# Performance work log

Measured on AMD Instinct MI355X. Metric: run time of the kernel, lower is better.

Reference implementation:

```python
import jax, jax.numpy as jnp
import numpy as np

B, T, V = 16, 512, 10000
E, H = 300, 256


def setup_inputs() -> dict:
    key = jax.random.key(0)
    ks = jax.random.split(key, 6)
    return {
        "input": jax.random.normal(ks[0], (B, T, V), dtype=jnp.float32),
        "hidden": jax.random.normal(ks[1], (B, H), dtype=jnp.float32),
        "W_emb": jax.random.normal(ks[2], (E, V), dtype=jnp.float32) * 0.02,
        "W_w": jax.random.normal(ks[3], (H, E), dtype=jnp.float32) * 0.05,
        "W_u": jax.random.normal(ks[4], (H, H), dtype=jnp.float32) * 0.05,
        "W_v": jax.random.normal(ks[5], (V, H), dtype=jnp.float32) * 0.05,
    }


def reference(input, hidden, W_emb, W_w, W_u, W_v):
    # Elman-style cell WITHOUT nonlinearity on the hidden state (matches source):
    #   e = x_t @ W_emb^T ; h = e @ W_w^T + h_prev @ W_u^T ; out = softmax(h @ W_v^T)
    def step(h, x_t):  # x_t: [B, V], h: [B, H]
        e = x_t @ W_emb.T                      # [B, E]
        h_new = e @ W_w.T + h @ W_u.T          # [B, H]
        out = jax.nn.softmax(h_new @ W_v.T, axis=1)  # [B, V]
        return h_new, out

    xs = jnp.swapaxes(input, 0, 1)             # [T, B, V]
    _, outs = jax.lax.scan(step, hidden, xs)   # outs: [T, B, V]
    return jnp.swapaxes(outs, 0, 1)            # [B, T, V]
```

## Files before the change

### kernel.cpp

```cpp
#include <hip/hip_runtime.h>

typedef __bf16 bf16x8 __attribute__((ext_vector_type(8)));
typedef float f32x4 __attribute__((ext_vector_type(4)));
typedef unsigned short u16x8 __attribute__((ext_vector_type(8)));

#define VP 10016

__device__ __forceinline__ unsigned short f2bf(float x){
  unsigned u = __builtin_bit_cast(unsigned, x);
  u += 0x7fffu + ((u>>16)&1u);
  return (unsigned short)(u>>16);
}
__device__ __forceinline__ float bf2f(unsigned short h){
  unsigned u = ((unsigned)h)<<16;
  return __builtin_bit_cast(float, u);
}

__global__ __launch_bounds__(256) void k_wvf(const float* __restrict__ W_v,
                                             unsigned short* __restrict__ Wvf,
                                             const float* __restrict__ W_u,
                                             unsigned short* __restrict__ Wu_bf){
  if(blockIdx.x >= 160){
    int i = (blockIdx.x-160)*256 + threadIdx.x;
    const float4 v = *(const float4*)(W_u + (size_t)i*4);
    unsigned a = (unsigned)f2bf(v.x) | ((unsigned)f2bf(v.y)<<16);
    unsigned b = (unsigned)f2bf(v.z) | ((unsigned)f2bf(v.w)<<16);
    *(uint2*)(Wu_bf + (size_t)i*4) = make_uint2(a,b);
    return;
  }
  const int t = threadIdx.x;
  const int w = t>>6, lane = t&63;
  const int l15 = lane&15, sl = lane>>4;
  const int vg = blockIdx.x*4 + w;
  const int v = vg*16 + l15;
  #pragma unroll
  for(int kk=0;kk<8;kk++){
    u16x8 pk = {0,0,0,0,0,0,0,0};
    if(v < 10000){
      const float* p = W_v + (size_t)v*256 + kk*32 + sl*8;
      float4 v0 = *(const float4*)p;
      float4 v1 = *(const float4*)(p+4);
      pk[0]=f2bf(v0.x); pk[1]=f2bf(v0.y); pk[2]=f2bf(v0.z); pk[3]=f2bf(v0.w);
      pk[4]=f2bf(v1.x); pk[5]=f2bf(v1.y); pk[6]=f2bf(v1.z); pk[7]=f2bf(v1.w);
    }
    *(u16x8*)(Wvf + ((size_t)vg*8 + kk)*512 + lane*8) = pk;
  }
}

__global__ __launch_bounds__(256) void k_m1(const float* __restrict__ W_w,
                                            const float* __restrict__ W_emb,
                                            unsigned short* __restrict__ M1f){
  __shared__ float4 ww4[16][75];
  const int t = threadIdx.x;
  const int ngrp = blockIdx.y;
  const int n0 = ngrp*16;
  for(int i=t; i<16*75; i+=256){
    int n = i/75, c = i - n*75;
    ww4[n][c] = *(const float4*)(W_w + (size_t)(n0+n)*300 + c*4);
  }
  __syncthreads();
  const int v0 = blockIdx.x*512 + t*2;
  if(v0 >= VP) return;
  const int c  = v0>>5;
  const int sl = (v0>>3)&3;
  const int j  = v0&7;
  unsigned short* outp = M1f + (size_t)(ngrp*313 + c)*512 + sl*128 + j;
  if(v0 >= 10000){
    #pragma unroll
    for(int nn=0;nn<16;nn++) *(unsigned*)&outp[nn*8] = 0u;
    return;
  }
  float acc[16][2];
  #pragma unroll
  for(int nn=0;nn<16;nn++){ acc[nn][0]=0.f; acc[nn][1]=0.f; }
  #pragma unroll 2
  for(int cc=0;cc<75;cc++){
    const float* eb = W_emb + (size_t)(4*cc)*10000 + v0;
    float2 wv0 = *(const float2*)(eb);
    float2 wv1 = *(const float2*)(eb + 10000);
    float2 wv2 = *(const float2*)(eb + 20000);
    float2 wv3 = *(const float2*)(eb + 30000);
    #pragma unroll
    for(int nn=0;nn<16;nn++){
      float4 w = ww4[nn][cc];
      acc[nn][0] += w.x*wv0.x + w.y*wv1.x + w.z*wv2.x + w.w*wv3.x;
      acc[nn][1] += w.x*wv0.y + w.y*wv1.y + w.z*wv2.y + w.w*wv3.y;
    }
  }
  #pragma unroll
  for(int nn=0;nn<16;nn++){
    unsigned pk = (unsigned)f2bf(acc[nn][0]) | ((unsigned)f2bf(acc[nn][1])<<16);
    *(unsigned*)&outp[nn*8] = pk;
  }
}

__global__ __launch_bounds__(512, 4) void k_gemm_a(const float* __restrict__ x,
    const unsigned short* __restrict__ M1f, float* __restrict__ gp, int nsplit){
  __shared__ unsigned short As[32768];
  char* Ab = (char*)As;
  const int t = threadIdx.x;
  const int w = t>>6, lane = t&63;
  const int l15 = lane&15, sl = lane>>4;
  const int mh = w>>2, nq = w&3;
  const int r0 = blockIdx.x*128;
  const int kh = blockIdx.y;
  const int base = 313/nsplit, rem = 313%nsplit;
  const int c0 = kh*base + (kh<rem ? kh : rem);
  const int c1 = c0 + base + (kh<rem ? 1 : 0);

  const unsigned short* mbp[4];
  #pragma unroll
  for(int nt=0;nt<4;nt++)
    mbp[nt] = M1f + (size_t)(nq*4+nt)*313*512 + lane*8;

  f32x4 acc[4][4] = {};
  for(int cs=c0; cs<c1; cs+=8){
    const int cs_n = (c1-cs) < 8 ? (c1-cs) : 8;
    if(lane*4 < cs_n*32){
      const int kk = cs*32 + lane*4;
      const bool ok = (kk + 4 <= 10000);
      const int unit0 = lane>>1;
      const int half8 = (lane&1)*8;
      const float* xp = x + (size_t)(r0 + w*16)*10000 + kk;
      #pragma unroll
      for(int g=0; g<2; g++){
        float4 rX[8];
        #pragma unroll
        for(int j=0;j<8;j++)
          rX[j] = ok ? *(const float4*)(xp + (size_t)(g*8+j)*10000)
                     : float4{0.f,0.f,0.f,0.f};
        #pragma unroll
        for(int j=0;j<8;j++){
          const int r = w*16 + g*8 + j;
          unsigned lo = (unsigned)f2bf(rX[j].x) | ((unsigned)f2bf(rX[j].y)<<16);
          unsigned hi = (unsigned)f2bf(rX[j].z) | ((unsigned)f2bf(rX[j].w)<<16);
          *(uint2*)(Ab + r*512 + (((lane>>1) ^ (r&7))<<4) + half8) = make_uint2(lo,hi);
        }
      }
      (void)unit0;
    }
    __syncthreads();
    for(int cc=0; cc<cs_n; cc++){
      const int c = cs + cc;
      bf16x8 b[4];
      #pragma unroll
      for(int nt=0;nt<4;nt++)
        b[nt] = *(const bf16x8*)(mbp[nt] + (size_t)c*512);
      bf16x8 a[4];
      #pragma unroll
      for(int mt=0;mt<4;mt++){
        const int r = mh*64 + mt*16 + l15;
        const int p = (cc*4 + sl) ^ (l15&7);
        a[mt] = *(const bf16x8*)(Ab + r*512 + p*16);
      }
      #pragma unroll
      for(int mt=0;mt<4;mt++)
        #pragma unroll
        for(int nt=0;nt<4;nt++)
          acc[mt][nt] = __builtin_amdgcn_mfma_f32_16x16x32_bf16(a[mt], b[nt], acc[mt][nt], 0,0,0);
    }
    __syncthreads();
  }

  float* gout = gp + (size_t)kh*2097152;
  #pragma unroll
  for(int mt=0;mt<4;mt++)
    #pragma unroll
    for(int nt=0;nt<4;nt++)
      #pragma unroll
      for(int i2=0;i2<4;i2++){
        int row = r0 + mh*64 + mt*16 + sl*4 + i2;
        int col = nq*64 + nt*16 + l15;
        gout[(size_t)row*256 + col] = acc[mt][nt][i2];
      }
}

__global__ __launch_bounds__(256) void k_reduce(float* __restrict__ gp, int nsplit){
  size_t i = ((size_t)blockIdx.x*256 + threadIdx.x)*4;
  float4 acc = *(const float4*)(gp + i);
  for(int s=1;s<nsplit;s++){
    const float4 v = *(const float4*)(gp + (size_t)s*2097152 + i);
    acc.x+=v.x; acc.y+=v.y; acc.z+=v.z; acc.w+=v.w;
  }
  *(float4*)(gp + i) = acc;
}

__global__ __launch_bounds__(256) void k_matsq(const float* __restrict__ A,
    const float* __restrict__ B, float* __restrict__ C){
  int i = blockIdx.x, j = threadIdx.x;
  __shared__ float arow[256];
  arow[j] = A[i*256 + j];
  __syncthreads();
  float acc = 0.f;
  for(int k=0;k<256;k++) acc += arow[k]*B[k*256 + j];
  C[i*256 + j] = acc;
}

__global__ __launch_bounds__(256) void k_scan_local(const float* __restrict__ g,
    const unsigned short* __restrict__ Wu, float* __restrict__ u_final){
  __shared__ unsigned short ub[2][16*256];
  const int m = blockIdx.x;
  const int t = threadIdx.x, wave=t>>6, lane=t&63, l15=lane&15, sl=lane>>4;
  for(int i=t;i<2048;i+=256) ((unsigned*)ub[0])[i] = 0u;
  __syncthreads();
  int buf = 0;
  for(int j=0;j<16;j++){
    float gv[4][4];
    #pragma unroll
    for(int nt=0;nt<4;nt++)
      #pragma unroll
      for(int i=0;i<4;i++){
        int b = sl*4 + i;
        int n = wave*64 + nt*16 + l15;
        size_t r = (size_t)b*512 + m*16 + j;
        gv[nt][i] = g[r*256 + n];
      }
    bf16x8 af[8];
    #pragma unroll
    for(int kk=0;kk<8;kk++){
      int slot = kk*4 + sl;
      af[kk] = *(const bf16x8*)&ub[buf][l15*256 + ((slot ^ (l15&7))<<3)];
    }
    f32x4 acc[4] = {};
    #pragma unroll
    for(int kk=0;kk<8;kk++)
      #pragma unroll
      for(int nt=0;nt<4;nt++){
        int n = wave*64 + nt*16 + l15;
        bf16x8 bv = *(const bf16x8*)&Wu[(size_t)n*256 + kk*32 + sl*8];
        acc[nt] = __builtin_amdgcn_mfma_f32_16x16x32_bf16(af[kk], bv, acc[nt], 0,0,0);
      }
    #pragma unroll
    for(int nt=0;nt<4;nt++)
      #pragma unroll
      for(int i=0;i<4;i++){
        int b = sl*4 + i;
        int n = wave*64 + nt*16 + l15;
        float v = acc[nt][i] + gv[nt][i];
        ub[buf^1][b*256 + (((n>>3) ^ (b&7))<<3) + (n&7)] = f2bf(v);
        if(j==15) u_final[m*4096 + b*256 + n] = v;
      }
    __syncthreads();
    buf ^= 1;
  }
}

__global__ __launch_bounds__(1024) void k_chunk_scan(const float* __restrict__ hidden,
    const float* __restrict__ u_final, const float* __restrict__ A16,
    float* __restrict__ h_start){
  const int b = blockIdx.x;
  const int t = threadIdx.x;
  const int n = t & 255, q = t >> 8;
  __shared__ float hc[256];
  __shared__ float part[3][256];
  float a[64];
  const float* ap = A16 + (size_t)n*256 + q*64;
  #pragma unroll
  for(int i=0;i<16;i++){
    float4 v = *(const float4*)(ap + i*4);
    a[i*4]=v.x; a[i*4+1]=v.y; a[i*4+2]=v.z; a[i*4+3]=v.w;
  }
  if(q==0){
    float h = hidden[b*256 + n];
    hc[n] = h;
    h_start[b*256 + n] = h;
  }
  __syncthreads();
  for(int m=1;m<32;m++){
    float acc0=0.f, acc1=0.f;
    #pragma unroll
    for(int i=0;i<64;i+=2){
      acc0 += a[i]  *hc[q*64 + i];
      acc1 += a[i+1]*hc[q*64 + i+1];
    }
    float acc = acc0 + acc1;
    if(q) part[q-1][n] = acc;
    __syncthreads();
    if(q==0){
      float v = acc + part[0][n] + part[1][n] + part[2][n]
              + u_final[(size_t)(m-1)*4096 + b*256 + n];
      hc[n] = v;
      h_start[(size_t)m*4096 + b*256 + n] = v;
    }
    __syncthreads();
  }
}

__global__ __launch_bounds__(256) void k_scan_fix(const float* __restrict__ g,
    const unsigned short* __restrict__ Wu, const float* __restrict__ h_start,
    unsigned short* __restrict__ h_bf){
  __shared__ unsigned short ub[2][16*256];
  const int m = blockIdx.x;
  const int t=threadIdx.x, wave=t>>6, lane=t&63, l15=lane&15, sl=lane>>4;
  for(int u=t; u<512; u+=256){
    int b = u>>5, s = u&31;
    const float* hp = h_start + m*4096 + b*256 + s*8;
    float4 v0 = *(const float4*)hp;
    float4 v1 = *(const float4*)(hp+4);
    u16x8 pk;
    pk[0]=f2bf(v0.x); pk[1]=f2bf(v0.y); pk[2]=f2bf(v0.z); pk[3]=f2bf(v0.w);
    pk[4]=f2bf(v1.x); pk[5]=f2bf(v1.y); pk[6]=f2bf(v1.z); pk[7]=f2bf(v1.w);
    *(u16x8*)&ub[0][b*256 + ((s ^ (b&7))<<3)] = pk;
  }
  __syncthreads();
  int buf = 0;
  for(int j=0;j<16;j++){
    float gv[4][4];
    #pragma unroll
    for(int nt=0;nt<4;nt++)
      #pragma unroll
      for(int i=0;i<4;i++){
        int b = sl*4 + i;
        int n = wave*64 + nt*16 + l15;
        size_t r = (size_t)b*512 + m*16 + j;
        gv[nt][i] = g[r*256 + n];
      }
    bf16x8 af[8];
    #pragma unroll
    for(int kk=0;kk<8;kk++){
      int slot = kk*4 + sl;
      af[kk] = *(const bf16x8*)&ub[buf][l15*256 + ((slot ^ (l15&7))<<3)];
    }
    f32x4 acc[4] = {};
    #pragma unroll
    for(int kk=0;kk<8;kk++)
      #pragma unroll
      for(int nt=0;nt<4;nt++){
        int n = wave*64 + nt*16 + l15;
        bf16x8 bv = *(const bf16x8*)&Wu[(size_t)n*256 + kk*32 + sl*8];
        acc[nt] = __builtin_amdgcn_mfma_f32_16x16x32_bf16(af[kk], bv, acc[nt], 0,0,0);
      }
    #pragma unroll
    for(int nt=0;nt<4;nt++)
      #pragma unroll
      for(int i=0;i<4;i++){
        int b = sl*4 + i;
        int n = wave*64 + nt*16 + l15;
        float v = acc[nt][i] + gv[nt][i];
        unsigned short hb = f2bf(v);
        ub[buf^1][b*256 + (((n>>3) ^ (b&7))<<3) + (n&7)] = hb;
        size_t r = (size_t)b*512 + m*16 + j;
        h_bf[r*256 + n] = hb;
      }
    __syncthreads();
    buf ^= 1;
  }
}

__global__ __launch_bounds__(512, 2) void k_gemm_c(const unsigned short* __restrict__ h_bf,
    const unsigned short* __restrict__ Wvf, char* __restrict__ out){
  const int t = threadIdx.x;
  const int w = t>>6, lane = t&63;
  const int l15 = lane&15, sl = lane>>4;
  const int mh = w>>2, nq = w&3;
  const int vt = blockIdx.x;

  const unsigned short* bp[4];
  #pragma unroll
  for(int nt=0;nt<4;nt++)
    bp[nt] = Wvf + (size_t)(vt*16 + nq*4 + nt)*8*512 + lane*8;

  bf16x8 ball[8][4];
  #pragma unroll
  for(int kk=0;kk<8;kk++)
    #pragma unroll
    for(int nt=0;nt<4;nt++)
      ball[kk][nt] = *(const bf16x8*)(bp[nt] + (size_t)kk*512);

  #pragma unroll
  for(int band=0; band<2; band++){
    const int rg = blockIdx.y + band*32;
    const int rbase = rg*128 + mh*64;
    f32x4 acc[4][4] = {};
    #pragma unroll
    for(int kk=0;kk<8;kk++){
      bf16x8 a[4];
      #pragma unroll
      for(int mt=0;mt<4;mt++)
        a[mt] = *(const bf16x8*)&h_bf[(size_t)(rbase + mt*16 + l15)*256 + kk*32 + sl*8];
      #pragma unroll
      for(int mt=0;mt<4;mt++)
        #pragma unroll
        for(int nt=0;nt<4;nt++)
          acc[mt][nt] = __builtin_amdgcn_mfma_f32_16x16x32_bf16(a[mt], ball[kk][nt], acc[mt][nt], 0,0,0);
    }
    #pragma unroll
    for(int mt=0;mt<4;mt++)
      #pragma unroll
      for(int nt=0;nt<4;nt++){
        const int v = vt*256 + (nq*4+nt)*16 + l15;
        if(v < 10000){
          #pragma unroll
          for(int i=0;i<4;i++){
            int row = rbase + mt*16 + sl*4 + i;
            *(unsigned short*)(out + (size_t)row*40000 + (size_t)v*2) = f2bf(acc[mt][nt][i]);
          }
        }
      }
  }
}

__global__ __launch_bounds__(256) void k_softmax(char* __restrict__ out){
  const int r = blockIdx.x;
  const int t = threadIdx.x;
  const unsigned short* lg = (const unsigned short*)(out + (size_t)r*40000);
  float vals[40];
  float mx = -3.0e38f;
  #pragma unroll
  for(int j=0;j<5;j++){
    int c = j*256 + t;
    if(c < 1250){
      u16x8 p = *(const u16x8*)(lg + (size_t)c*8);
      #pragma unroll
      for(int q=0;q<8;q++){
        float a = bf2f(p[q]);
        vals[j*8+q] = a;
        mx = fmaxf(mx, a);
      }
    }
  }
  #pragma unroll
  for(int o=32;o>=1;o>>=1) mx = fmaxf(mx, __shfl_xor(mx, o));
  __shared__ float redm[4], reds[4];
  if((t&63)==0) redm[t>>6] = mx;
  __syncthreads();
  mx = fmaxf(fmaxf(redm[0],redm[1]), fmaxf(redm[2],redm[3]));
  float s = 0.f;
  #pragma unroll
  for(int j=0;j<5;j++){
    int c = j*256 + t;
    if(c < 1250){
      #pragma unroll
      for(int q=0;q<8;q++){
        float e = __expf(vals[j*8+q]-mx);
        vals[j*8+q] = e;
        s += e;
      }
    }
  }
  #pragma unroll
  for(int o=32;o>=1;o>>=1) s += __shfl_xor(s, o);
  if((t&63)==0) reds[t>>6] = s;
  __syncthreads();
  s = reds[0]+reds[1]+reds[2]+reds[3];
  float inv = 1.0f/s;
  float* op = (float*)(out + (size_t)r*40000);
  #pragma unroll
  for(int j=0;j<5;j++){
    int c = j*256 + t;
    if(c < 1250){
      float4 s0, s1;
      s0.x=vals[j*8+0]*inv; s0.y=vals[j*8+1]*inv; s0.z=vals[j*8+2]*inv; s0.w=vals[j*8+3]*inv;
      s1.x=vals[j*8+4]*inv; s1.y=vals[j*8+5]*inv; s1.z=vals[j*8+6]*inv; s1.w=vals[j*8+7]*inv;
      *(float4*)(op + (size_t)c*8)     = s0;
      *(float4*)(op + (size_t)c*8 + 4) = s1;
    }
  }
}

extern "C" void kernel_launch(void* const* d_in, const int* in_sizes, int n_in,
                              void* d_out, int out_size, void* d_ws, size_t ws_size,
                              hipStream_t stream){
  const float* x      = (const float*)d_in[0];
  const float* hidden = (const float*)d_in[1];
  const float* W_emb  = (const float*)d_in[2];
  const float* W_w    = (const float*)d_in[3];
  const float* W_u    = (const float*)d_in[4];
  const float* W_v    = (const float*)d_in[5];

  const size_t fixed_bytes = 16269312;
  int nsplit = 2;
  if(ws_size >= (size_t)8*2097152*4 + fixed_bytes) nsplit = 8;
  else if(ws_size >= (size_t)4*2097152*4 + fixed_bytes) nsplit = 4;

  char* w = (char*)d_ws;
  size_t off = (size_t)nsplit * 2097152 * 4;
  float*          gp      = (float*)(w + 0);
  unsigned short* M1f     = (unsigned short*)(w + off);          off += 5128192;
  unsigned short* Wvf     = (unsigned short*)(w + off);          off += 5242880;
  unsigned short* Wu_bf   = (unsigned short*)(w + off);          off += 131072;
  float*          u_final = (float*)(w + off);                   off += 524288;
  float*          h_start = (float*)(w + off);                   off += 524288;
  unsigned short* h_bf    = (unsigned short*)(w + off);          off += 4194304;
  float*          powA    = (float*)(w + off);                   off += 262144;
  float*          powB    = (float*)(w + off);                   off += 262144;

  k_m1<<<dim3(20,16),256,0,stream>>>(W_w, W_emb, M1f);
  k_gemm_a<<<dim3(64,nsplit),512,0,stream>>>(x, M1f, gp, nsplit);
  k_wvf<<<224,256,0,stream>>>(W_v, Wvf, W_u, Wu_bf);
  k_matsq<<<256,256,0,stream>>>(W_u,  W_u,  powA);
  k_matsq<<<256,256,0,stream>>>(powA, powA, powB);
  k_matsq<<<256,256,0,stream>>>(powB, powB, powA);
  k_matsq<<<256,256,0,stream>>>(powA, powA, powB);
  k_reduce<<<2048,256,0,stream>>>(gp, nsplit);
  k_scan_local<<<32,256,0,stream>>>(gp, Wu_bf, u_final);
  k_chunk_scan<<<16,1024,0,stream>>>(hidden, u_final, powB, h_start);
  k_scan_fix<<<32,256,0,stream>>>(gp, Wu_bf, h_start, h_bf);
  k_gemm_c<<<dim3(40,32),512,0,stream>>>(h_bf, Wvf, (char*)d_out);
  k_softmax<<<8192,256,0,stream>>>((char*)d_out);
}
```

Before: 509.4 us.

## Double-buffer A tile in k_gemm_a with register prefetch of next chunk

Switches the GEMM's shared-memory A tile from one 8-chunk buffer to two 4-chunk buffers. Global loads for the next half-step are issued into registers before the MFMA loop over the current buffer, then converted and written to the alternate buffer. This removes one barrier per iteration and overlaps global-load latency with compute. The cost is twice as many loop iterations with smaller steps and more live registers, which may pressure occupancy at the 512x4 launch bound.

```diff
diff --git a/kernel.cpp b/kernel.cpp
--- a/kernel.cpp
+++ b/kernel.cpp
@@ -96,8 +96,7 @@
 
 __global__ __launch_bounds__(512, 4) void k_gemm_a(const float* __restrict__ x,
     const unsigned short* __restrict__ M1f, float* __restrict__ gp, int nsplit){
-  __shared__ unsigned short As[32768];
-  char* Ab = (char*)As;
+  __shared__ unsigned short As[2][16384];
   const int t = threadIdx.x;
   const int w = t>>6, lane = t&63;
   const int l15 = lane&15, sl = lane>>4;
@@ -113,35 +112,53 @@
   for(int nt=0;nt<4;nt++)
     mbp[nt] = M1f + (size_t)(nq*4+nt)*313*512 + lane*8;
 
+  const int lhalf = lane>>5, lcol = lane&31;
+  const float* xrow = x + (size_t)(r0 + w*16)*10000;
+  float4 rX[8];
+
+  auto LOADG = [&](int ch, int hn){
+    if(lcol < hn*8){
+      const int kk = ch*32 + lcol*4;
+      const bool ok = (kk + 4 <= 10000);
+      #pragma unroll
+      for(int jj=0;jj<8;jj++)
+        rX[jj] = ok ? *(const float4*)(xrow + (size_t)(2*jj+lhalf)*10000 + kk)
+                    : float4{0.f,0.f,0.f,0.f};
+    }
+  };
+  auto WRITEG = [&](int hn, int bufi){
+    if(lcol < hn*8){
+      char* Ab = (char*)As[bufi];
+      #pragma unroll
+      for(int jj=0;jj<8;jj++){
+        const int r = w*16 + 2*jj + lhalf;
+        unsigned lo = (unsigned)f2bf(rX[jj].x) | ((unsigned)f2bf(rX[jj].y)<<16);
+        unsigned hi = (unsigned)f2bf(rX[jj].z) | ((unsigned)f2bf(rX[jj].w)<<16);
+        *(uint2*)(Ab + r*256 + (((lcol>>1) ^ (r&7))<<4) + (lcol&1)*8) = make_uint2(lo,hi);
+      }
+    }
+  };
+
   f32x4 acc[4][4] = {};
-  for(int cs=c0; cs<c1; cs+=8){
-    const int cs_n = (c1-cs) < 8 ? (c1-cs) : 8;
-    if(lane*4 < cs_n*32){
-      const int kk = cs*32 + lane*4;
-      const bool ok = (kk + 4 <= 10000);
-      const int unit0 = lane>>1;
-      const int half8 = (lane&1)*8;
-      const float* xp = x + (size_t)(r0 + w*16)*10000 + kk;
-      #pragma unroll
-      for(int g=0; g<2; g++){
-        float4 rX[8];
-        #pragma unroll
-        for(int j=0;j<8;j++)
-          rX[j] = ok ? *(const float4*)(xp + (size_t)(g*8+j)*10000)
-                     : float4{0.f,0.f,0.f,0.f};
-        #pragma unroll
-        for(int j=0;j<8;j++){
-          const int r = w*16 + g*8 + j;
-          unsigned lo = (unsigned)f2bf(rX[j].x) | ((unsigned)f2bf(rX[j].y)<<16);
-          unsigned hi = (unsigned)f2bf(rX[j].z) | ((unsigned)f2bf(rX[j].w)<<16);
-          *(uint2*)(Ab + r*512 + (((lane>>1) ^ (r&7))<<4) + half8) = make_uint2(lo,hi);
-        }
-      }
-      (void)unit0;
-    }
+
+  const int nhalf = (c1 - c0 + 3) >> 2;
+  {
+    const int hn0 = (c1-c0) < 4 ? (c1-c0) : 4;
+    LOADG(c0, hn0);
+    WRITEG(hn0, 0);
+  }
+
+  int hb = 0;
+  for(int hs=0; hs<nhalf; hs++){
+    const int ch = c0 + hs*4;
+    const int hn = (c1-ch) < 4 ? (c1-ch) : 4;
+    const int ch2 = ch + 4;
+    const int hn2 = (hs+1 < nhalf) ? ((c1-ch2) < 4 ? (c1-ch2) : 4) : 0;
     __syncthreads();
-    for(int cc=0; cc<cs_n; cc++){
-      const int c = cs + cc;
+    if(hn2) LOADG(ch2, hn2);
+    const char* Ab = (const char*)As[hb];
+    for(int cc=0; cc<hn; cc++){
+      const int c = ch + cc;
       bf16x8 b[4];
       #pragma unroll
       for(int nt=0;nt<4;nt++)
@@ -151,7 +168,7 @@
       for(int mt=0;mt<4;mt++){
         const int r = mh*64 + mt*16 + l15;
         const int p = (cc*4 + sl) ^ (l15&7);
-        a[mt] = *(const bf16x8*)(Ab + r*512 + p*16);
+        a[mt] = *(const bf16x8*)(Ab + r*256 + p*16);
       }
       #pragma unroll
       for(int mt=0;mt<4;mt++)
@@ -159,7 +176,8 @@
         for(int nt=0;nt<4;nt++)
           acc[mt][nt] = __builtin_amdgcn_mfma_f32_16x16x32_bf16(a[mt], b[nt], acc[mt][nt], 0,0,0);
     }
-    __syncthreads();
+    if(hn2) WRITEG(hn2, hb^1);
+    hb ^= 1;
   }
 
   float* gout = gp + (size_t)kh*2097152;
```

New measurement: 594.9 us. +16.8%, slower.
